# Performance work log

Hardware: AMD Instinct MI355X
Metric: run time of the kernel (lower is better)

The kernel has to match this reference:

```python
import jax, jax.numpy as jnp
import numpy as np

B_, S_, D_, N_, R_ = 2, 2048, 1024, 16, 64  # batch, seq, d_model, d_state, dt_rank


def setup_inputs() -> dict:
    key = jax.random.key(0)
    ks = jax.random.split(key, 12)
    x = jax.random.normal(ks[0], (B_, S_, D_), dtype=jnp.float32)
    # params (xavier-ish scale)
    W_dtw = jax.random.normal(ks[1], (R_, D_), dtype=jnp.float32) * (1.0 / np.sqrt(D_))
    W_dt = jax.random.normal(ks[2], (D_, R_), dtype=jnp.float32) * (1.0 / np.sqrt(R_))
    b_dt = jnp.zeros((D_,), dtype=jnp.float32)
    A_log = jnp.log(jax.random.uniform(ks[3], (D_, N_), minval=0.5, maxval=1.5, dtype=jnp.float32))
    W_B = jax.random.normal(ks[4], (N_, D_), dtype=jnp.float32) * (1.0 / np.sqrt(D_))
    W_C = jax.random.normal(ks[5], (N_, D_), dtype=jnp.float32) * (1.0 / np.sqrt(D_))
    Dp = jnp.ones((D_,), dtype=jnp.float32)
    ln_g = jnp.ones((D_,), dtype=jnp.float32)
    ln_b = jnp.zeros((D_,), dtype=jnp.float32)
    W_out = jax.random.normal(ks[6], (D_, D_), dtype=jnp.float32) * (1.0 / np.sqrt(D_))
    return {"x": x, "W_dtw": W_dtw, "W_dt": W_dt, "b_dt": b_dt, "A_log": A_log,
            "W_B": W_B, "W_C": W_C, "Dp": Dp, "ln_g": ln_g, "ln_b": ln_b, "W_out": W_out}


def _layernorm(y, g, b, eps=1e-5):
    mu = jnp.mean(y, axis=-1, keepdims=True)
    var = jnp.mean(jnp.square(y - mu), axis=-1, keepdims=True)
    return (y - mu) * jax.lax.rsqrt(var + eps) * g + b


def reference(x, W_dtw, W_dt, b_dt, A_log, W_B, W_C, Dp, ln_g, ln_b, W_out):
    # projections
    dt = jnp.einsum('bsd,rd->bsr', x, W_dtw)                 # [B,S,R]
    delta = jax.nn.softplus(jnp.einsum('bsr,dr->bsd', dt, W_dt) + b_dt)  # [B,S,D]
    Bm = jnp.einsum('bsd,nd->bsn', x, W_B)                   # [B,S,N]
    Cm = jnp.einsum('bsd,nd->bsn', x, W_C)                   # [B,S,N]
    A = -jnp.exp(A_log)                                      # [D,N]

    def step(h, inp):
        d_t, b_t, c_t, x_t = inp                             # [B,D],[B,N],[B,N],[B,D]
        dA = jnp.exp(d_t[..., None] * A)                     # [B,D,N]
        h = dA * h + (d_t[..., None] * b_t[:, None, :]) * x_t[..., None]
        y_t = jnp.sum(h * c_t[:, None, :], axis=-1)          # [B,D]
        return h, y_t

    h0 = jnp.zeros((x.shape[0], x.shape[2], A.shape[1]), dtype=x.dtype)
    xs = (jnp.swapaxes(delta, 0, 1), jnp.swapaxes(Bm, 0, 1),
          jnp.swapaxes(Cm, 0, 1), jnp.swapaxes(x, 0, 1))
    _, ys = jax.lax.scan(step, h0, xs)                       # ys: [S,B,D]
    y = jnp.swapaxes(ys, 0, 1) + Dp * x                      # [B,S,D]
    y = _layernorm(y, ln_g, ln_b)
    return jnp.einsum('bsd,ed->bse', y, W_out)
```

## Files before the change

### kernel.cpp

```cpp
#include <hip/hip_runtime.h>
#include <hip/hip_bf16.h>

#define B_ 2
#define S_ 2048
#define D_ 1024
#define N_ 16
#define R_ 64
#define NC 64
#define CL 32
#define BS_ (B_*S_)
#define KSPLIT 8

typedef __attribute__((ext_vector_type(4))) float f32x4;
typedef __attribute__((ext_vector_type(8))) short bf16x8;
typedef __attribute__((ext_vector_type(8))) unsigned short u16x8;

__device__ __forceinline__ unsigned short f2b(float v) {
  unsigned u = __builtin_bit_cast(unsigned, v);
  unsigned r = ((u >> 16) & 1u) + 0x7FFFu;
  return (unsigned short)((u + r) >> 16);
}

__device__ __forceinline__ void gload_lds16(const void* g, void* l) {
  __builtin_amdgcn_global_load_lds(
      (const __attribute__((address_space(1))) unsigned int*)g,
      (__attribute__((address_space(3))) unsigned int*)l, 16, 0, 0);
}

__global__ __launch_bounds__(256) void k_castall(
    const float* __restrict__ x, const float* __restrict__ W_dtw,
    const float* __restrict__ W_B, const float* __restrict__ W_C,
    const float* __restrict__ W_dt, const float* __restrict__ W_out,
    unsigned short* __restrict__ xb, unsigned short* __restrict__ Wcat,
    unsigned short* __restrict__ wdtb, unsigned short* __restrict__ wob) {
  int i = (blockIdx.x * 256 + threadIdx.x) * 4;
  const float* s; unsigned short* d; int off;
  if (i < 4194304)      { s = x;     d = xb;           off = 0; }
  else if (i < 4259840) { s = W_dtw; d = Wcat;         off = 4194304; }
  else if (i < 4276224) { s = W_B;   d = Wcat + 65536; off = 4259840; }
  else if (i < 4292608) { s = W_C;   d = Wcat + 81920; off = 4276224; }
  else if (i < 4358144) { s = W_dt;  d = wdtb;         off = 4292608; }
  else                  { s = W_out; d = wob;          off = 4358144; }
  int j = i - off;
  float4 v = *(const float4*)&s[j];
  ushort4 o;
  o.x = f2b(v.x); o.y = f2b(v.y); o.z = f2b(v.z); o.w = f2b(v.w);
  *(ushort4*)&d[j] = o;
}

__global__ __launch_bounds__(256, 2) void k_proj(
    const unsigned short* __restrict__ xb, const unsigned short* __restrict__ Wcat,
    float* __restrict__ part) {
  __shared__ __align__(16) unsigned short Xs[2][64 * 64];
  __shared__ __align__(16) unsigned short Ws[2][96 * 64];
  const int tid = threadIdx.x;
  const int lane = tid & 63, w = tid >> 6;
  const size_t row0 = (size_t)blockIdx.x * 64;
  const int kbase = blockIdx.y * (D_ / KSPLIT);
  f32x4 acc[6] = {};

  auto stage = [&](int buf, int k0) {
    #pragma unroll
    for (int i = 0; i < 2; ++i) {
      int id = i * 256 + tid; int row = id >> 3, s = id & 7;
      gload_lds16(xb + (row0 + row) * D_ + k0 + ((s ^ (row & 7)) << 3),
                  Xs[buf] + row * 64 + s * 8);
    }
    #pragma unroll
    for (int i = 0; i < 3; ++i) {
      int id = i * 256 + tid; int row = id >> 3, s = id & 7;
      gload_lds16(Wcat + (size_t)row * D_ + k0 + ((s ^ (row & 7)) << 3),
                  Ws[buf] + row * 64 + s * 8);
    }
  };
  stage(0, kbase);
  __syncthreads();
  int cur = 0;
  const int r = lane & 15, kg = lane >> 4;
  for (int t = 0; t < 2; ++t) {
    if (t < 1) stage(cur ^ 1, kbase + 64);
    #pragma unroll
    for (int ks = 0; ks < 2; ++ks) {
      const int arow = w * 16 + r;
      bf16x8 a = *(const bf16x8*)&Xs[cur][arow * 64 + ((((ks << 2) | kg) ^ (arow & 7)) << 3)];
      #pragma unroll
      for (int nt = 0; nt < 6; ++nt) {
        const int brow = nt * 16 + r;
        bf16x8 b = *(const bf16x8*)&Ws[cur][brow * 64 + ((((ks << 2) | kg) ^ (brow & 7)) << 3)];
        acc[nt] = __builtin_amdgcn_mfma_f32_16x16x32_bf16(a, b, acc[nt], 0, 0, 0);
      }
    }
    __syncthreads();
    cur ^= 1;
  }
  const int cr = lane >> 4, cc = lane & 15;
  float* pb = part + (size_t)blockIdx.y * (BS_ * 96);
  #pragma unroll
  for (int nt = 0; nt < 6; ++nt)
    #pragma unroll
    for (int j = 0; j < 4; ++j)
      pb[(row0 + w * 16 + cr * 4 + j) * 96 + nt * 16 + cc] = acc[nt][j];
}

__global__ __launch_bounds__(256) void k_projred(
    const float* __restrict__ part, unsigned short* __restrict__ dtb,
    float* __restrict__ Bm, float* __restrict__ Cm) {
  int e = blockIdx.x * 256 + threadIdx.x;
  int row = e / 96, col = e - row * 96;
  float s = 0.f;
  #pragma unroll
  for (int p = 0; p < KSPLIT; ++p) s += part[e + (size_t)p * (BS_ * 96)];
  if (col < 64)      dtb[row * R_ + col] = f2b(s);
  else if (col < 80) Bm[row * N_ + col - 64] = s;
  else               Cm[row * N_ + col - 80] = s;
}

__global__ __launch_bounds__(256) void k_delta(
    const unsigned short* __restrict__ dtb, const unsigned short* __restrict__ wdtb,
    const float* __restrict__ b_dt, float* __restrict__ delta) {
  __shared__ __align__(16) unsigned short As[128 * 64];
  __shared__ __align__(16) unsigned short Bs[128 * 64];
  const int tid = threadIdx.x;
  const int lane = tid & 63, wid = tid >> 6;
  const int wr = wid >> 1, wc = wid & 1;
  const size_t row0 = (size_t)blockIdx.x * 128;
  const size_t col0 = (size_t)blockIdx.y * 128;
  f32x4 acc[4][4] = {};

  {
    const int r = tid >> 3, s = tid & 7;
    #pragma unroll
    for (int i = 0; i < 4; ++i) {
      const int row = i * 32 + r;
      const int gs = s ^ (row & 7);
      gload_lds16(dtb + (row0 + row) * R_ + gs * 8, As + row * 64 + s * 8);
      gload_lds16(wdtb + (col0 + row) * R_ + gs * 8, Bs + row * 64 + s * 8);
    }
  }
  __syncthreads();
  const int r = lane & 15, kg = lane >> 4;
  #pragma unroll
  for (int ks = 0; ks < 2; ++ks) {
    bf16x8 a[4], b[4];
    #pragma unroll
    for (int m = 0; m < 4; ++m) {
      const int arow = wr * 64 + m * 16 + r;
      a[m] = *(const bf16x8*)&As[arow * 64 + (((ks << 2) | kg) ^ (arow & 7)) * 8];
    }
    #pragma unroll
    for (int n = 0; n < 4; ++n) {
      const int brow = wc * 64 + n * 16 + r;
      b[n] = *(const bf16x8*)&Bs[brow * 64 + (((ks << 2) | kg) ^ (brow & 7)) * 8];
    }
    #pragma unroll
    for (int m = 0; m < 4; ++m)
      #pragma unroll
      for (int n = 0; n < 4; ++n)
        acc[m][n] = __builtin_amdgcn_mfma_f32_16x16x32_bf16(a[m], b[n], acc[m][n], 0, 0, 0);
  }
  const int cr = lane >> 4, cc = lane & 15;
  #pragma unroll
  for (int m = 0; m < 4; ++m) {
    #pragma unroll
    for (int n = 0; n < 4; ++n) {
      const int d = (int)col0 + wc * 64 + n * 16 + cc;
      const float bd = b_dt[d];
      #pragma unroll
      for (int j = 0; j < 4; ++j) {
        size_t trow = row0 + wr * 64 + m * 16 + cr * 4 + j;
        float v = acc[m][n][j] + bd;
        float sp = fmaxf(v, 0.f) + log1pf(__expf(-fabsf(v)));
        delta[trow * D_ + d] = sp;
      }
    }
  }
}

__global__ __launch_bounds__(256) void k_scan1(
    const float* __restrict__ x, const float* __restrict__ delta,
    const float* __restrict__ Bm, const float* __restrict__ A_log,
    float* __restrict__ aprod, float* __restrict__ hend) {
  int g = blockIdx.x * 256 + threadIdx.x;
  int nq = g & 3;
  int d = (g >> 2) & (D_ - 1);
  int c = (g >> 12) & (NC - 1);
  int b = g >> 18;

  float4 av = *(const float4*)&A_log[(size_t)d * N_ + nq * 4];
  float Ad[4] = {-__expf(av.x), -__expf(av.y), -__expf(av.z), -__expf(av.w)};
  float ap[4] = {1.f, 1.f, 1.f, 1.f}, h[4] = {0.f, 0.f, 0.f, 0.f};

  size_t base = (size_t)(b * S_ + c * CL) * D_ + d;
  size_t bcb  = (size_t)(b * S_ + c * CL) * N_ + nq * 4;
  for (int s = 0; s < CL; ++s) {
    float dlt = delta[base + (size_t)s * D_];
    float xv  = x[base + (size_t)s * D_];
    float dbx = dlt * xv;
    float4 Bv = *(const float4*)&Bm[bcb + (size_t)s * N_];
    float da0 = __expf(dlt * Ad[0]), da1 = __expf(dlt * Ad[1]);
    float da2 = __expf(dlt * Ad[2]), da3 = __expf(dlt * Ad[3]);
    ap[0] *= da0; ap[1] *= da1; ap[2] *= da2; ap[3] *= da3;
    h[0] = da0 * h[0] + dbx * Bv.x;
    h[1] = da1 * h[1] + dbx * Bv.y;
    h[2] = da2 * h[2] + dbx * Bv.z;
    h[3] = da3 * h[3] + dbx * Bv.w;
  }
  size_t o = (((size_t)(b * NC + c)) * D_ + d) * N_ + nq * 4;
  *(float4*)&aprod[o] = make_float4(ap[0], ap[1], ap[2], ap[3]);
  *(float4*)&hend[o]  = make_float4(h[0], h[1], h[2], h[3]);
}

__global__ __launch_bounds__(256) void k_scan2(
    const float* __restrict__ aprod, const float* __restrict__ hend,
    float* __restrict__ hstart) {
  int g = blockIdx.x * 256 + threadIdx.x;
  int n = g & (N_ - 1);
  int d = (g >> 4) & (D_ - 1);
  int b = g >> 14;
  float h = 0.f;
  for (int c = 0; c < NC; ++c) {
    size_t idx = (((size_t)b * NC + c) * D_ + d) * N_ + n;
    hstart[idx] = h;
    h = aprod[idx] * h + hend[idx];
  }
}

__global__ __launch_bounds__(256) void k_scan3(
    const float* __restrict__ x, const float* __restrict__ delta,
    const float* __restrict__ Bm, const float* __restrict__ Cm,
    const float* __restrict__ A_log, const float* __restrict__ hstart,
    const float* __restrict__ Dp, float* __restrict__ ypre) {
  int g = blockIdx.x * 256 + threadIdx.x;
  int nq = g & 3;
  int d = (g >> 2) & (D_ - 1);
  int c = (g >> 12) & (NC - 1);
  int b = g >> 18;

  float4 av = *(const float4*)&A_log[(size_t)d * N_ + nq * 4];
  float Ad[4] = {-__expf(av.x), -__expf(av.y), -__expf(av.z), -__expf(av.w)};
  float h[4];
  {
    size_t o = (((size_t)(b * NC + c)) * D_ + d) * N_ + nq * 4;
    float4 v = *(const float4*)&hstart[o];
    h[0] = v.x; h[1] = v.y; h[2] = v.z; h[3] = v.w;
  }
  const float Dpd = Dp[d];

  size_t base = (size_t)(b * S_ + c * CL) * D_ + d;
  size_t bcb  = (size_t)(b * S_ + c * CL) * N_ + nq * 4;
  for (int s = 0; s < CL; ++s) {
    float dlt = delta[base + (size_t)s * D_];
    float xv  = x[base + (size_t)s * D_];
    float dbx = dlt * xv;
    float4 Bv = *(const float4*)&Bm[bcb + (size_t)s * N_];
    float4 Cv = *(const float4*)&Cm[bcb + (size_t)s * N_];
    float da0 = __expf(dlt * Ad[0]), da1 = __expf(dlt * Ad[1]);
    float da2 = __expf(dlt * Ad[2]), da3 = __expf(dlt * Ad[3]);
    h[0] = da0 * h[0] + dbx * Bv.x;
    h[1] = da1 * h[1] + dbx * Bv.y;
    h[2] = da2 * h[2] + dbx * Bv.z;
    h[3] = da3 * h[3] + dbx * Bv.w;
    float y = h[0] * Cv.x + h[1] * Cv.y + h[2] * Cv.z + h[3] * Cv.w;
    y += __shfl_xor(y, 1);
    y += __shfl_xor(y, 2);
    if (nq == 0) ypre[base + (size_t)s * D_] = y + Dpd * xv;
  }
}

__device__ __forceinline__ float block_sum256(float v, float* sm) {
  #pragma unroll
  for (int o = 32; o > 0; o >>= 1) v += __shfl_down(v, o, 64);
  int w = threadIdx.x >> 6;
  __syncthreads();
  if ((threadIdx.x & 63) == 0) sm[w] = v;
  __syncthreads();
  return (sm[0] + sm[1]) + (sm[2] + sm[3]);
}

__global__ __launch_bounds__(256) void k_ln(
    const float* __restrict__ ypre, const float* __restrict__ g,
    const float* __restrict__ bta, unsigned short* __restrict__ ybf) {
  __shared__ float sm[4];
  const int t = blockIdx.x;
  const int tid = threadIdx.x;
  size_t base = (size_t)t * D_ + tid * 4;
  float4 v = *(const float4*)&ypre[base];
  float s1 = block_sum256(v.x + v.y + v.z + v.w, sm);
  float mu = s1 * (1.f / D_);
  float cx = v.x - mu, cy = v.y - mu, cz = v.z - mu, cw = v.w - mu;
  float s2 = block_sum256(cx*cx + cy*cy + cz*cz + cw*cw, sm);
  float rs = rsqrtf(s2 * (1.f / D_) + 1e-5f);
  float4 gg = *(const float4*)&g[tid * 4];
  float4 bb = *(const float4*)&bta[tid * 4];
  ushort4 o;
  o.x = f2b(cx * rs * gg.x + bb.x);
  o.y = f2b(cy * rs * gg.y + bb.y);
  o.z = f2b(cz * rs * gg.z + bb.z);
  o.w = f2b(cw * rs * gg.w + bb.w);
  *(ushort4*)&ybf[base] = o;
}

__device__ __forceinline__ void stage128x64(const unsigned short* __restrict__ g,
                                            size_t row0, int k0,
                                            unsigned short* lds, int tid) {
  const int r = tid >> 3, s = tid & 7;
  #pragma unroll
  for (int i = 0; i < 4; ++i) {
    const int row = i * 32 + r;
    const int gs = s ^ (row & 7);
    gload_lds16(g + ((row0 + row) << 10) + k0 + (gs << 3), lds + row * 64 + s * 8);
  }
}

__device__ __forceinline__ void stage64x64(const unsigned short* __restrict__ g,
                                           size_t row0, int k0,
                                           unsigned short* lds, int tid) {
  const int r = tid >> 3, s = tid & 7;
  #pragma unroll
  for (int i = 0; i < 2; ++i) {
    const int row = i * 32 + r;
    const int gs = s ^ (row & 7);
    gload_lds16(g + ((row0 + row) << 10) + k0 + (gs << 3), lds + row * 64 + s * 8);
  }
}

__global__ __launch_bounds__(256, 2) void k_out(const unsigned short* __restrict__ Y,
                                                const unsigned short* __restrict__ W,
                                                float* __restrict__ O) {
  __shared__ __align__(16) unsigned short As[2][128 * 64];
  __shared__ __align__(16) unsigned short Bs[2][64 * 64];
  const int tid = threadIdx.x;
  const int lane = tid & 63, wid = tid >> 6;
  const size_t row0 = (size_t)blockIdx.x * 128;
  const size_t col0 = (size_t)blockIdx.y * 64;
  f32x4 acc[2][4] = {};

  stage128x64(Y, row0, 0, As[0], tid);
  stage64x64(W, col0, 0, Bs[0], tid);
  __syncthreads();

  int cur = 0;
  const int r = lane & 15, kg = lane >> 4;
  for (int t = 0; t < 16; ++t) {
    if (t + 1 < 16) {
      stage128x64(Y, row0, (t + 1) * 64, As[cur ^ 1], tid);
      stage64x64(W, col0, (t + 1) * 64, Bs[cur ^ 1], tid);
    }
    #pragma unroll
    for (int ks = 0; ks < 2; ++ks) {
      bf16x8 a[2], b[4];
      #pragma unroll
      for (int m = 0; m < 2; ++m) {
        const int arow = wid * 32 + m * 16 + r;
        a[m] = *(const bf16x8*)&As[cur][arow * 64 + (((ks << 2) | kg) ^ (arow & 7)) * 8];
      }
      #pragma unroll
      for (int n = 0; n < 4; ++n) {
        const int brow = n * 16 + r;
        b[n] = *(const bf16x8*)&Bs[cur][brow * 64 + (((ks << 2) | kg) ^ (brow & 7)) * 8];
      }
      #pragma unroll
      for (int m = 0; m < 2; ++m)
        #pragma unroll
        for (int n = 0; n < 4; ++n)
          acc[m][n] = __builtin_amdgcn_mfma_f32_16x16x32_bf16(a[m], b[n], acc[m][n], 0, 0, 0);
    }
    __syncthreads();
    cur ^= 1;
  }

  const int cr = lane >> 4, cc = lane & 15;
  #pragma unroll
  for (int m = 0; m < 2; ++m) {
    #pragma unroll
    for (int n = 0; n < 4; ++n) {
      size_t orow = row0 + wid * 32 + m * 16 + cr * 4;
      float* op = O + orow * D_ + col0 + n * 16 + cc;
      #pragma unroll
      for (int j = 0; j < 4; ++j) op[(size_t)j * D_] = acc[m][n][j];
    }
  }
}

extern "C" void kernel_launch(void* const* d_in, const int* in_sizes, int n_in,
                              void* d_out, int out_size, void* d_ws, size_t ws_size,
                              hipStream_t stream) {
  const float* x     = (const float*)d_in[0];
  const float* W_dtw = (const float*)d_in[1];
  const float* W_dt  = (const float*)d_in[2];
  const float* b_dt  = (const float*)d_in[3];
  const float* A_log = (const float*)d_in[4];
  const float* W_B   = (const float*)d_in[5];
  const float* W_C   = (const float*)d_in[6];
  const float* Dp    = (const float*)d_in[7];
  const float* ln_g  = (const float*)d_in[8];
  const float* ln_b  = (const float*)d_in[9];
  const float* W_out = (const float*)d_in[10];
  float* out = (float*)d_out;

  float* ws = (float*)d_ws;
  float* delta  = ws;
  float* ypre   = delta  + (size_t)BS_ * D_;
  float* Bm     = ypre   + (size_t)BS_ * D_;
  float* Cm     = Bm     + (size_t)BS_ * N_;
  float* aprod  = Cm     + (size_t)BS_ * N_;
  float* hend   = aprod  + (size_t)B_ * NC * D_ * N_;
  float* hstart = hend   + (size_t)B_ * NC * D_ * N_;
  float* part   = hstart + (size_t)B_ * NC * D_ * N_;
  unsigned short* xb   = (unsigned short*)(part + (size_t)KSPLIT * BS_ * 96);
  unsigned short* Wcat = xb   + (size_t)BS_ * D_;
  unsigned short* wdtb = Wcat + (size_t)96 * D_;
  unsigned short* wob  = wdtb + (size_t)D_ * R_;
  unsigned short* ybf  = wob  + (size_t)D_ * D_;
  unsigned short* dtb  = ybf  + (size_t)BS_ * D_;

  k_castall<<<dim3(5280), dim3(256), 0, stream>>>(x, W_dtw, W_B, W_C, W_dt, W_out,
                                                  xb, Wcat, wdtb, wob);
  k_proj<<<dim3(BS_ / 64, KSPLIT), dim3(256), 0, stream>>>(xb, Wcat, part);
  k_projred<<<dim3(BS_ * 96 / 256), dim3(256), 0, stream>>>(part, dtb, Bm, Cm);
  k_delta<<<dim3(BS_ / 128, D_ / 128), dim3(256), 0, stream>>>(dtb, wdtb, b_dt, delta);
  k_scan1<<<dim3(B_ * NC * D_ * 4 / 256), dim3(256), 0, stream>>>(x, delta, Bm, A_log,
                                                                  aprod, hend);
  k_scan2<<<dim3(B_ * D_ * N_ / 256), dim3(256), 0, stream>>>(aprod, hend, hstart);
  k_scan3<<<dim3(B_ * NC * D_ * 4 / 256), dim3(256), 0, stream>>>(x, delta, Bm, Cm,
                                                                  A_log, hstart, Dp, ypre);
  k_ln<<<dim3(BS_), dim3(256), 0, stream>>>(ypre, ln_g, ln_b, ybf);
  k_out<<<dim3(BS_ / 128, D_ / 64), dim3(256), 0, stream>>>(ybf, wob, out);
}
```

Baseline: 114.9 us.

## Fuse x bf16 cast into projection and stage scan inputs through LDS

Removes the separate fp32-to-bf16 cast pass over x by converting on the fly inside the projection kernel's staging loads. It also restructures the two chunked scan kernels so each block covers 64 channels of one chunk, loads delta, x, B and C tiles into shared memory with async global-to-LDS copies, and writes the output through shared memory as coalesced vector stores. This targets the strided per-thread global loads and the extra read and write of x. In exchange, k_proj's x loads become synchronous register loads and are no longer async LDS copies, and each projection K-split block now converts x again.

```diff
diff --git a/kernel.cpp b/kernel.cpp
--- a/kernel.cpp
+++ b/kernel.cpp
@@ -28,19 +28,18 @@
 }
 
 __global__ __launch_bounds__(256) void k_castall(
-    const float* __restrict__ x, const float* __restrict__ W_dtw,
-    const float* __restrict__ W_B, const float* __restrict__ W_C,
-    const float* __restrict__ W_dt, const float* __restrict__ W_out,
-    unsigned short* __restrict__ xb, unsigned short* __restrict__ Wcat,
-    unsigned short* __restrict__ wdtb, unsigned short* __restrict__ wob) {
+    const float* __restrict__ W_dtw, const float* __restrict__ W_B,
+    const float* __restrict__ W_C, const float* __restrict__ W_dt,
+    const float* __restrict__ W_out,
+    unsigned short* __restrict__ Wcat, unsigned short* __restrict__ wdtb,
+    unsigned short* __restrict__ wob) {
   int i = (blockIdx.x * 256 + threadIdx.x) * 4;
   const float* s; unsigned short* d; int off;
-  if (i < 4194304)      { s = x;     d = xb;           off = 0; }
-  else if (i < 4259840) { s = W_dtw; d = Wcat;         off = 4194304; }
-  else if (i < 4276224) { s = W_B;   d = Wcat + 65536; off = 4259840; }
-  else if (i < 4292608) { s = W_C;   d = Wcat + 81920; off = 4276224; }
-  else if (i < 4358144) { s = W_dt;  d = wdtb;         off = 4292608; }
-  else                  { s = W_out; d = wob;          off = 4358144; }
+  if (i < 65536)       { s = W_dtw; d = Wcat;         off = 0; }
+  else if (i < 81920)  { s = W_B;   d = Wcat + 65536; off = 65536; }
+  else if (i < 98304)  { s = W_C;   d = Wcat + 81920; off = 81920; }
+  else if (i < 163840) { s = W_dt;  d = wdtb;         off = 98304; }
+  else                 { s = W_out; d = wob;          off = 163840; }
   int j = i - off;
   float4 v = *(const float4*)&s[j];
   ushort4 o;
@@ -49,7 +48,7 @@
 }
 
 __global__ __launch_bounds__(256, 2) void k_proj(
-    const unsigned short* __restrict__ xb, const unsigned short* __restrict__ Wcat,
+    const float* __restrict__ x, const unsigned short* __restrict__ Wcat,
     float* __restrict__ part) {
   __shared__ __align__(16) unsigned short Xs[2][64 * 64];
   __shared__ __align__(16) unsigned short Ws[2][96 * 64];
@@ -63,8 +62,13 @@
     #pragma unroll
     for (int i = 0; i < 2; ++i) {
       int id = i * 256 + tid; int row = id >> 3, s = id & 7;
-      gload_lds16(xb + (row0 + row) * D_ + k0 + ((s ^ (row & 7)) << 3),
-                  Xs[buf] + row * 64 + s * 8);
+      const float* gp = &x[(row0 + row) * D_ + k0 + s * 8];
+      float4 v0 = *(const float4*)gp;
+      float4 v1 = *(const float4*)(gp + 4);
+      u16x8 u;
+      u[0] = f2b(v0.x); u[1] = f2b(v0.y); u[2] = f2b(v0.z); u[3] = f2b(v0.w);
+      u[4] = f2b(v1.x); u[5] = f2b(v1.y); u[6] = f2b(v1.z); u[7] = f2b(v1.w);
+      *(u16x8*)&Xs[buf][row * 64 + ((s ^ (row & 7)) << 3)] = u;
     }
     #pragma unroll
     for (int i = 0; i < 3; ++i) {
@@ -180,34 +184,53 @@
     const float* __restrict__ x, const float* __restrict__ delta,
     const float* __restrict__ Bm, const float* __restrict__ A_log,
     float* __restrict__ aprod, float* __restrict__ hend) {
-  int g = blockIdx.x * 256 + threadIdx.x;
-  int nq = g & 3;
-  int d = (g >> 2) & (D_ - 1);
-  int c = (g >> 12) & (NC - 1);
-  int b = g >> 18;
-
+  __shared__ __align__(16) float sd[CL][64];
+  __shared__ __align__(16) float sx[CL][64];
+  __shared__ __align__(16) float sB[CL][N_];
+  const int tid = threadIdx.x;
+  const int db = blockIdx.x & 15;
+  const int c  = (blockIdx.x >> 4) & (NC - 1);
+  const int b  = blockIdx.x >> 10;
+  const int d0 = db * 64;
+  const size_t tokbase = (size_t)(b * S_ + c * CL);
+
+  {
+    int s = tid >> 4, jf = (tid & 15) * 4;
+    size_t g = (tokbase + s) * D_ + d0 + jf;
+    gload_lds16(&delta[g], &sd[s][jf]);
+    gload_lds16(&x[g],     &sx[s][jf]);
+    gload_lds16(&delta[g + (size_t)16 * D_], &sd[s + 16][jf]);
+    gload_lds16(&x[g + (size_t)16 * D_],     &sx[s + 16][jf]);
+    if (tid < 128) {
+      int s2 = tid >> 2, nf = (tid & 3) * 4;
+      gload_lds16(&Bm[(tokbase + s2) * N_ + nf], &sB[s2][nf]);
+    }
+  }
+  const int nq = tid & 3, dl = tid >> 2;
+  const int d = d0 + dl;
   float4 av = *(const float4*)&A_log[(size_t)d * N_ + nq * 4];
-  float Ad[4] = {-__expf(av.x), -__expf(av.y), -__expf(av.z), -__expf(av.w)};
-  float ap[4] = {1.f, 1.f, 1.f, 1.f}, h[4] = {0.f, 0.f, 0.f, 0.f};
-
-  size_t base = (size_t)(b * S_ + c * CL) * D_ + d;
-  size_t bcb  = (size_t)(b * S_ + c * CL) * N_ + nq * 4;
+  float Ad0 = -__expf(av.x), Ad1 = -__expf(av.y);
+  float Ad2 = -__expf(av.z), Ad3 = -__expf(av.w);
+  __syncthreads();
+
+  float ap0 = 1.f, ap1 = 1.f, ap2 = 1.f, ap3 = 1.f;
+  float h0 = 0.f, h1 = 0.f, h2 = 0.f, h3 = 0.f;
+  #pragma unroll 8
   for (int s = 0; s < CL; ++s) {
-    float dlt = delta[base + (size_t)s * D_];
-    float xv  = x[base + (size_t)s * D_];
-    float dbx = dlt * xv;
-    float4 Bv = *(const float4*)&Bm[bcb + (size_t)s * N_];
-    float da0 = __expf(dlt * Ad[0]), da1 = __expf(dlt * Ad[1]);
-    float da2 = __expf(dlt * Ad[2]), da3 = __expf(dlt * Ad[3]);
-    ap[0] *= da0; ap[1] *= da1; ap[2] *= da2; ap[3] *= da3;
-    h[0] = da0 * h[0] + dbx * Bv.x;
-    h[1] = da1 * h[1] + dbx * Bv.y;
-    h[2] = da2 * h[2] + dbx * Bv.z;
-    h[3] = da3 * h[3] + dbx * Bv.w;
+    float dlt = sd[s][dl];
+    float dbx = dlt * sx[s][dl];
+    float4 Bv = *(const float4*)&sB[s][nq * 4];
+    float da0 = __expf(dlt * Ad0), da1 = __expf(dlt * Ad1);
+    float da2 = __expf(dlt * Ad2), da3 = __expf(dlt * Ad3);
+    ap0 *= da0; ap1 *= da1; ap2 *= da2; ap3 *= da3;
+    h0 = da0 * h0 + dbx * Bv.x;
+    h1 = da1 * h1 + dbx * Bv.y;
+    h2 = da2 * h2 + dbx * Bv.z;
+    h3 = da3 * h3 + dbx * Bv.w;
   }
   size_t o = (((size_t)(b * NC + c)) * D_ + d) * N_ + nq * 4;
-  *(float4*)&aprod[o] = make_float4(ap[0], ap[1], ap[2], ap[3]);
-  *(float4*)&hend[o]  = make_float4(h[0], h[1], h[2], h[3]);
+  *(float4*)&aprod[o] = make_float4(ap0, ap1, ap2, ap3);
+  *(float4*)&hend[o]  = make_float4(h0, h1, h2, h3);
 }
 
 __global__ __launch_bounds__(256) void k_scan2(
@@ -230,40 +253,69 @@
     const float* __restrict__ Bm, const float* __restrict__ Cm,
     const float* __restrict__ A_log, const float* __restrict__ hstart,
     const float* __restrict__ Dp, float* __restrict__ ypre) {
-  int g = blockIdx.x * 256 + threadIdx.x;
-  int nq = g & 3;
-  int d = (g >> 2) & (D_ - 1);
-  int c = (g >> 12) & (NC - 1);
-  int b = g >> 18;
-
+  __shared__ __align__(16) float sd[CL][64];
+  __shared__ __align__(16) float sx[CL][64];
+  __shared__ __align__(16) float sB[CL][N_];
+  __shared__ __align__(16) float sC[CL][N_];
+  __shared__ __align__(16) float sy[CL][64];
+  const int tid = threadIdx.x;
+  const int db = blockIdx.x & 15;
+  const int c  = (blockIdx.x >> 4) & (NC - 1);
+  const int b  = blockIdx.x >> 10;
+  const int d0 = db * 64;
+  const size_t tokbase = (size_t)(b * S_ + c * CL);
+
+  {
+    int s = tid >> 4, jf = (tid & 15) * 4;
+    size_t g = (tokbase + s) * D_ + d0 + jf;
+    gload_lds16(&delta[g], &sd[s][jf]);
+    gload_lds16(&x[g],     &sx[s][jf]);
+    gload_lds16(&delta[g + (size_t)16 * D_], &sd[s + 16][jf]);
+    gload_lds16(&x[g + (size_t)16 * D_],     &sx[s + 16][jf]);
+    if (tid < 128) {
+      int s2 = tid >> 2, nf = (tid & 3) * 4;
+      gload_lds16(&Bm[(tokbase + s2) * N_ + nf], &sB[s2][nf]);
+      gload_lds16(&Cm[(tokbase + s2) * N_ + nf], &sC[s2][nf]);
+    }
+  }
+  const int nq = tid & 3, dl = tid >> 2;
+  const int d = d0 + dl;
   float4 av = *(const float4*)&A_log[(size_t)d * N_ + nq * 4];
-  float Ad[4] = {-__expf(av.x), -__expf(av.y), -__expf(av.z), -__expf(av.w)};
-  float h[4];
+  float Ad0 = -__expf(av.x), Ad1 = -__expf(av.y);
+  float Ad2 = -__expf(av.z), Ad3 = -__expf(av.w);
+  float h0, h1, h2, h3;
   {
     size_t o = (((size_t)(b * NC + c)) * D_ + d) * N_ + nq * 4;
     float4 v = *(const float4*)&hstart[o];
-    h[0] = v.x; h[1] = v.y; h[2] = v.z; h[3] = v.w;
+    h0 = v.x; h1 = v.y; h2 = v.z; h3 = v.w;
   }
   const float Dpd = Dp[d];
-
-  size_t base = (size_t)(b * S_ + c * CL) * D_ + d;
-  size_t bcb  = (size_t)(b * S_ + c * CL) * N_ + nq * 4;
+  __syncthreads();
+
+  #pragma unroll 8
   for (int s = 0; s < CL; ++s) {
-    float dlt = delta[base + (size_t)s * D_];
-    float xv  = x[base + (size_t)s * D_];
+    float dlt = sd[s][dl];
+    float xv  = sx[s][dl];
     float dbx = dlt * xv;
-    float4 Bv = *(const float4*)&Bm[bcb + (size_t)s * N_];
-    float4 Cv = *(const float4*)&Cm[bcb + (size_t)s * N_];
-    float da0 = __expf(dlt * Ad[0]), da1 = __expf(dlt * Ad[1]);
-    float da2 = __expf(dlt * Ad[2]), da3 = __expf(dlt * Ad[3]);
-    h[0] = da0 * h[0] + dbx * Bv.x;
-    h[1] = da1 * h[1] + dbx * Bv.y;
-    h[2] = da2 * h[2] + dbx * Bv.z;
-    h[3] = da3 * h[3] + dbx * Bv.w;
-    float y = h[0] * Cv.x + h[1] * Cv.y + h[2] * Cv.z + h[3] * Cv.w;
+    float4 Bv = *(const float4*)&sB[s][nq * 4];
+    float4 Cv = *(const float4*)&sC[s][nq * 4];
+    float da0 = __expf(dlt * Ad0), da1 = __expf(dlt * Ad1);
+    float da2 = __expf(dlt * Ad2), da3 = __expf(dlt * Ad3);
+    h0 = da0 * h0 + dbx * Bv.x;
+    h1 = da1 * h1 + dbx * Bv.y;
+    h2 = da2 * h2 + dbx * Bv.z;
+    h3 = da3 * h3 + dbx * Bv.w;
+    float y = h0 * Cv.x + h1 * Cv.y + h2 * Cv.z + h3 * Cv.w;
     y += __shfl_xor(y, 1);
     y += __shfl_xor(y, 2);
-    if (nq == 0) ypre[base + (size_t)s * D_] = y + Dpd * xv;
+    if (nq == 0) sy[s][dl] = y + Dpd * xv;
+  }
+  __syncthreads();
+  {
+    int s = tid >> 3, j = (tid & 7) * 8;
+    size_t g = (tokbase + s) * D_ + d0 + j;
+    *(float4*)&ypre[g]     = *(float4*)&sy[s][j];
+    *(float4*)&ypre[g + 4] = *(float4*)&sy[s][j + 4];
   }
 }
 
@@ -407,23 +459,22 @@
   float* hend   = aprod  + (size_t)B_ * NC * D_ * N_;
   float* hstart = hend   + (size_t)B_ * NC * D_ * N_;
   float* part   = hstart + (size_t)B_ * NC * D_ * N_;
-  unsigned short* xb   = (unsigned short*)(part + (size_t)KSPLIT * BS_ * 96);
-  unsigned short* Wcat = xb   + (size_t)BS_ * D_;
+  unsigned short* Wcat = (unsigned short*)(part + (size_t)KSPLIT * BS_ * 96);
   unsigned short* wdtb = Wcat + (size_t)96 * D_;
   unsigned short* wob  = wdtb + (size_t)D_ * R_;
   unsigned short* ybf  = wob  + (size_t)D_ * D_;
   unsigned short* dtb  = ybf  + (size_t)BS_ * D_;
 
-  k_castall<<<dim3(5280), dim3(256), 0, stream>>>(x, W_dtw, W_B, W_C, W_dt, W_out,
-                                                  xb, Wcat, wdtb, wob);
-  k_proj<<<dim3(BS_ / 64, KSPLIT), dim3(256), 0, stream>>>(xb, Wcat, part);
+  k_castall<<<dim3(1184), dim3(256), 0, stream>>>(W_dtw, W_B, W_C, W_dt, W_out,
+                                                  Wcat, wdtb, wob);
+  k_proj<<<dim3(BS_ / 64, KSPLIT), dim3(256), 0, stream>>>(x, Wcat, part);
   k_projred<<<dim3(BS_ * 96 / 256), dim3(256), 0, stream>>>(part, dtb, Bm, Cm);
   k_delta<<<dim3(BS_ / 128, D_ / 128), dim3(256), 0, stream>>>(dtb, wdtb, b_dt, delta);
-  k_scan1<<<dim3(B_ * NC * D_ * 4 / 256), dim3(256), 0, stream>>>(x, delta, Bm, A_log,
-                                                                  aprod, hend);
+  k_scan1<<<dim3(B_ * NC * (D_ / 64)), dim3(256), 0, stream>>>(x, delta, Bm, A_log,
+                                                               aprod, hend);
   k_scan2<<<dim3(B_ * D_ * N_ / 256), dim3(256), 0, stream>>>(aprod, hend, hstart);
-  k_scan3<<<dim3(B_ * NC * D_ * 4 / 256), dim3(256), 0, stream>>>(x, delta, Bm, Cm,
-                                                                  A_log, hstart, Dp, ypre);
+  k_scan3<<<dim3(B_ * NC * (D_ / 64)), dim3(256), 0, stream>>>(x, delta, Bm, Cm,
+                                                               A_log, hstart, Dp, ypre);
   k_ln<<<dim3(BS_), dim3(256), 0, stream>>>(ypre, ln_g, ln_b, ybf);
   k_out<<<dim3(BS_ / 128, D_ / 64), dim3(256), 0, stream>>>(ybf, wob, out);
 }
```

Result: faster. 110.6 us (-3.8%).
